# Performance work log

Measured on AMD Instinct MI355X. Metric: run time of the kernel, lower is better.

Reference implementation:

```python
import jax, jax.numpy as jnp
import numpy as np

N_NODES = 50000
N_EDGES = 500000
IN_DIM = 512
HID = 512


def setup_inputs() -> dict:
    key = jax.random.key(0)
    ks = jax.random.split(key, 12)
    s = 0.02  # weight init scale
    x = jax.random.normal(ks[0], (N_NODES, IN_DIM), dtype=jnp.float32)
    edge_index = jax.random.randint(ks[1], (2, N_EDGES), 0, N_NODES, dtype=jnp.int32)
    return {
        "x": x,
        "edge_index": edge_index,
        "Wl0": jax.random.normal(ks[2], (IN_DIM, HID), jnp.float32) * s,
        "bl0": jnp.zeros((HID,), jnp.float32),
        "Wr0": jax.random.normal(ks[3], (IN_DIM, HID), jnp.float32) * s,
        "Wl1": jax.random.normal(ks[4], (HID, HID), jnp.float32) * s,
        "bl1": jnp.zeros((HID,), jnp.float32),
        "Wr1": jax.random.normal(ks[5], (HID, HID), jnp.float32) * s,
        "Wv": jax.random.normal(ks[6], (HID, HID), jnp.float32) * s,
        "bv": jnp.zeros((HID,), jnp.float32),
        "Wt": jax.random.normal(ks[7], (HID, HID), jnp.float32) * s,
        "bt": jnp.zeros((HID,), jnp.float32),
    }


def _sage_conv(x, src, dst, Wl, bl, Wr, n_nodes):
    # mean-aggregate source features at target nodes, then dual linear
    msg_sum = jax.ops.segment_sum(x[src], dst, num_segments=n_nodes)  # [N, d]
    deg = jax.ops.segment_sum(jnp.ones_like(dst, dtype=x.dtype), dst, num_segments=n_nodes)
    mean = msg_sum / jnp.maximum(deg, 1.0)[:, None]
    return mean @ Wl + bl + x @ Wr


def reference(x, edge_index, Wl0, bl0, Wr0, Wl1, bl1, Wr1, Wv, bv, Wt, bt):
    n = x.shape[0]
    src, dst = edge_index[0], edge_index[1]
    h = _sage_conv(x, src, dst, Wl0, bl0, Wr0, n)
    h = jax.nn.relu(h)  # dropout is identity in eval mode
    h = _sage_conv(h, src, dst, Wl1, bl1, Wr1, n)
    x_vision = jax.nn.relu(h @ Wv + bv)
    x_text = jax.nn.relu(h @ Wt + bt)
    return (h, x_vision, x_text)
```

## Files before the change

kernel.cpp:

```cpp
#include <hip/hip_runtime.h>
#include <hip/hip_bf16.h>
#include <stdint.h>

#define N_NODES 50000
#define N_EDGES 500000
#define DIM 512

typedef unsigned short u16;
typedef unsigned int u32;
typedef __bf16 bf16x8 __attribute__((ext_vector_type(8)));
typedef float f32x4 __attribute__((ext_vector_type(4)));

static __device__ __forceinline__ u16 f2bf(float f) {
  union { __bf16 b; u16 u; } cv; cv.b = (__bf16)f; return cv.u;
}
static __device__ __forceinline__ float bf2f(u16 u) {
  union { u16 u; __bf16 b; } cv; cv.u = u; return (float)cv.b;
}

__global__ void k_zero(int4* __restrict__ deg4) {
  int t = blockIdx.x * 256 + threadIdx.x;
  if (t < 12500) deg4[t] = make_int4(0, 0, 0, 0);
}

__global__ __launch_bounds__(1024) void k_scan(const int* __restrict__ deg,
                                               int* __restrict__ offs,
                                               int* __restrict__ pos,
                                               float* __restrict__ invd) {
  __shared__ int sums[1024];
  const int tid = threadIdx.x;
  const int CH = 49;
  int lo = tid * CH;
  int hi = lo + CH; if (hi > N_NODES) hi = N_NODES;
  if (lo > N_NODES) lo = N_NODES;
  int s = 0;
  for (int i = lo; i < hi; ++i) s += deg[i];
  sums[tid] = s;
  __syncthreads();
  for (int off = 1; off < 1024; off <<= 1) {
    int t = (tid >= off) ? sums[tid - off] : 0;
    __syncthreads();
    sums[tid] += t;
    __syncthreads();
  }
  int run = sums[tid] - s;
  for (int i = lo; i < hi; ++i) {
    int d = deg[i];
    offs[i] = run; pos[i] = run;
    invd[i] = 1.0f / (float)((d > 1) ? d : 1);
    run += d;
  }
  if (tid == 1023) offs[N_NODES] = run;
}

__global__ void k_scatter(const int* __restrict__ src, const int* __restrict__ dst,
                          int* __restrict__ pos, int* __restrict__ srcs) {
  int e = blockIdx.x * blockDim.x + threadIdx.x;
  if (e < N_EDGES) {
    int p = atomicAdd(&pos[dst[e]], 1);
    srcs[p] = src[e] * DIM;
  }
}

__global__ __launch_bounds__(256) void k_prep(
    const float* __restrict__ x, u16* __restrict__ xb,
    const int* __restrict__ dst, int* __restrict__ deg,
    const float* __restrict__ Wa, const float* __restrict__ Wb,
    const float* __restrict__ Wc, const float* __restrict__ Wd,
    const float* __restrict__ We, const float* __restrict__ Wf,
    u16* __restrict__ Oa, u16* __restrict__ Ob, u16* __restrict__ Oc,
    u16* __restrict__ Od, u16* __restrict__ Oe, u16* __restrict__ Of) {
  __shared__ u16 tbuf[64][66];
  const int t = blockIdx.x * 256 + threadIdx.x;

  const float4* p = (const float4*)(x + (size_t)t * 8);
  float4 a = p[0], b = p[1];
  uint4 o;
  o.x = (u32)f2bf(a.x) | ((u32)f2bf(a.y) << 16);
  o.y = (u32)f2bf(a.z) | ((u32)f2bf(a.w) << 16);
  o.z = (u32)f2bf(b.x) | ((u32)f2bf(b.y) << 16);
  o.w = (u32)f2bf(b.z) | ((u32)f2bf(b.w) << 16);
  *(uint4*)(xb + (size_t)t * 8) = o;

  if (t < N_EDGES) atomicAdd(&deg[dst[t]], 1);

  const int wb = (int)blockIdx.x - (12500 - 384);
  if (wb >= 0) {
    const float* W; u16* O;
    switch (wb / 64) {
      case 0: W = Wa; O = Oa; break;
      case 1: W = Wb; O = Ob; break;
      case 2: W = Wc; O = Oc; break;
      case 3: W = Wd; O = Od; break;
      case 4: W = We; O = Oe; break;
      default: W = Wf; O = Of; break;
    }
    const int rem = wb & 63;
    const int k0 = (rem & 7) * 64, n0 = (rem >> 3) * 64;
    const int lr = threadIdx.x & 63, wr = threadIdx.x >> 6;
#pragma unroll
    for (int rr = 0; rr < 16; ++rr) {
      int k = k0 + wr * 16 + rr;
      tbuf[lr][wr * 16 + rr] = f2bf(W[(size_t)k * 512 + n0 + lr]);
    }
    __syncthreads();
#pragma unroll
    for (int rr = 0; rr < 16; ++rr) {
      int n = n0 + wr * 16 + rr;
      O[(size_t)n * 512 + k0 + lr] = tbuf[wr * 16 + rr][lr];
    }
  }
}

#define ACCB(A, q)                                              \
  A[0] += bf2f((q).x & 0xffff); A[1] += bf2f((u16)((q).x >> 16)); \
  A[2] += bf2f((q).y & 0xffff); A[3] += bf2f((u16)((q).y >> 16)); \
  A[4] += bf2f((q).z & 0xffff); A[5] += bf2f((u16)((q).z >> 16)); \
  A[6] += bf2f((q).w & 0xffff); A[7] += bf2f((u16)((q).w >> 16));

__global__ __launch_bounds__(256) void k_agg_bf16(
    const u16* __restrict__ hb, const int* __restrict__ offs,
    const int* __restrict__ srcs, const float* __restrict__ invd,
    u16* __restrict__ outb) {
  int node = blockIdx.x * 4 + (threadIdx.x >> 6);
  int lane = threadIdx.x & 63;
  if (node >= N_NODES) return;
  int s0 = offs[node], s1 = offs[node + 1];
  float acc[8] = {0, 0, 0, 0, 0, 0, 0, 0};
  float acd[8] = {0, 0, 0, 0, 0, 0, 0, 0};
  const u16* hl = hb + lane * 8;
  int i = s0;
  for (; i + 8 <= s1; i += 8) {
    int sa = srcs[i], sb = srcs[i + 1], sc = srcs[i + 2], sd = srcs[i + 3];
    int se = srcs[i + 4], sf = srcs[i + 5], sg = srcs[i + 6], sh = srcs[i + 7];
    uint4 qa = *(const uint4*)(hl + sa);
    uint4 qb = *(const uint4*)(hl + sb);
    uint4 qc = *(const uint4*)(hl + sc);
    uint4 qd = *(const uint4*)(hl + sd);
    uint4 qe = *(const uint4*)(hl + se);
    uint4 qf = *(const uint4*)(hl + sf);
    uint4 qg = *(const uint4*)(hl + sg);
    uint4 qh = *(const uint4*)(hl + sh);
    ACCB(acc, qa) ACCB(acd, qb) ACCB(acc, qc) ACCB(acd, qd)
    ACCB(acc, qe) ACCB(acd, qf) ACCB(acc, qg) ACCB(acd, qh)
  }
  if (i + 4 <= s1) {
    int sa = srcs[i], sb = srcs[i + 1], sc = srcs[i + 2], sd = srcs[i + 3];
    uint4 qa = *(const uint4*)(hl + sa);
    uint4 qb = *(const uint4*)(hl + sb);
    uint4 qc = *(const uint4*)(hl + sc);
    uint4 qd = *(const uint4*)(hl + sd);
    ACCB(acc, qa) ACCB(acd, qb) ACCB(acc, qc) ACCB(acd, qd)
    i += 4;
  }
  if (i + 2 <= s1) {
    int sa = srcs[i], sb = srcs[i + 1];
    uint4 qa = *(const uint4*)(hl + sa);
    uint4 qb = *(const uint4*)(hl + sb);
    ACCB(acc, qa) ACCB(acd, qb)
    i += 2;
  }
  if (i < s1) {
    int sa = srcs[i];
    uint4 qa = *(const uint4*)(hl + sa);
    ACCB(acc, qa)
  }
  float iv = invd[node];
#pragma unroll
  for (int k = 0; k < 8; ++k) acc[k] = (acc[k] + acd[k]) * iv;
  uint4 o;
  o.x = (u32)f2bf(acc[0]) | ((u32)f2bf(acc[1]) << 16);
  o.y = (u32)f2bf(acc[2]) | ((u32)f2bf(acc[3]) << 16);
  o.z = (u32)f2bf(acc[4]) | ((u32)f2bf(acc[5]) << 16);
  o.w = (u32)f2bf(acc[6]) | ((u32)f2bf(acc[7]) << 16);
  *(uint4*)(outb + (size_t)node * DIM + lane * 8) = o;
}

#define MFMA __builtin_amdgcn_mfma_f32_16x16x32_bf16
#define BUFU 39936

template <int EPI>
__global__ __launch_bounds__(512, 2) void k_gemm112(
    const u16* __restrict__ A1, const u16* __restrict__ W1,
    const u16* __restrict__ A2, const u16* __restrict__ W2,
    const float* __restrict__ bias, const float* __restrict__ bias2,
    float* __restrict__ outf, float* __restrict__ outf2,
    u16* __restrict__ outb, int NT) {
  __shared__ u16 lds[2 * BUFU];
  const int tid = threadIdx.x;
  const int wid = tid >> 6, lane = tid & 63;
  int head = 0, row0;
  if (EPI == 3) {
    head = (int)blockIdx.x & 1;
    row0 = ((int)blockIdx.x >> 1) * 112;
  } else {
    row0 = (int)blockIdx.x * 112;
  }
  const u16* BW = (EPI == 3) ? (head ? W2 : W1) : nullptr;

  f32x4 acc[7][4];
  const f32x4 z = {0.f, 0.f, 0.f, 0.f};
#pragma unroll
  for (int i = 0; i < 7; ++i)
#pragma unroll
    for (int j = 0; j < 4; ++j) acc[i][j] = z;

  const int ly = lane >> 3;
  const int schunk = (lane & 7) ^ ly;

  auto stageA = [&](int t, int h) {
    u16* tile = lds + (t & 1) * BUFU;
    const u16* G = (EPI == 3) ? A1 : ((t < 8) ? A1 : A2);
    int w = wid;
    if (h && w >= 6) w -= 2;
    const int rb = h * 64 + w * 8;
    int rg = row0 + rb + ly;
    if (rg > N_NODES - 1) rg = N_NODES - 1;
    const u16* g = G + (size_t)rg * 512 + (t & 7) * 64 + schunk * 8;
    __builtin_amdgcn_global_load_lds(
        (const __attribute__((address_space(1))) void*)g,
        (__attribute__((address_space(3))) void*)(tile + rb * 64), 16, 0, 0);
  };

  auto stageB = [&](int t, int jh) {
    u16* tile = lds + (t & 1) * BUFU + 7168;
    const u16* G = (EPI == 3) ? BW : ((t < 8) ? W1 : W2);
    const int kofs = (t & 7) * 64 + schunk * 8;
#pragma unroll
    for (int u = 0; u < 4; ++u) {
      const int rb = u * 128 + (wid >> 2) * 64 + (wid & 3) * 8 + jh * 32;
      const u16* g = G + (size_t)(rb + ly) * 512 + kofs;
      __builtin_amdgcn_global_load_lds(
          (const __attribute__((address_space(1))) void*)g,
          (__attribute__((address_space(3))) void*)(tile + rb * 64), 16, 0, 0);
    }
  };

  auto rdA = [&](const u16* T_, int ig, int kk) -> bf16x8 {
    const int r = ig * 16 + (lane & 15);
    const int off = ((kk * 4 + (lane >> 4)) ^ (lane & 7)) * 8;
    return *(const bf16x8*)(T_ + r * 64 + off);
  };
  auto rdB = [&](const u16* T_, int jg, int kk) -> bf16x8 {
    const int r = wid * 64 + jg * 16 + (lane & 15);
    const int off = ((kk * 4 + (lane >> 4)) ^ (lane & 7)) * 8;
    return *(const bf16x8*)(T_ + r * 64 + off);
  };

  stageA(0, 0); stageB(0, 0); stageB(0, 1); stageA(0, 1);

  for (int t = 0; t < NT; ++t) {
    const u16* At = lds + (t & 1) * BUFU;
    const u16* Bt = At + 7168;
    const bool more = (t + 1 < NT);
    bf16x8 aF[4][2], bF[2][2];

    asm volatile("s_waitcnt vmcnt(5)" ::: "memory");
    __builtin_amdgcn_s_barrier();
    asm volatile("" ::: "memory");
    if (more) stageA(t + 1, 0);
#pragma unroll
    for (int ip = 0; ip < 4; ++ip)
#pragma unroll
      for (int kk = 0; kk < 2; ++kk) aF[ip][kk] = rdA(At, ip, kk);
#pragma unroll
    for (int jp = 0; jp < 2; ++jp)
#pragma unroll
      for (int kk = 0; kk < 2; ++kk) bF[jp][kk] = rdB(Bt, jp, kk);
    __builtin_amdgcn_s_setprio(1);
#pragma unroll
    for (int ip = 0; ip < 4; ++ip)
#pragma unroll
      for (int jp = 0; jp < 2; ++jp)
#pragma unroll
        for (int kk = 0; kk < 2; ++kk)
          acc[ip][jp] = MFMA(aF[ip][kk], bF[jp][kk], acc[ip][jp], 0, 0, 0);
    __builtin_amdgcn_s_setprio(0);

    if (more) { asm volatile("s_waitcnt vmcnt(1)" ::: "memory"); }
    else      { asm volatile("s_waitcnt vmcnt(0)" ::: "memory"); }
    __builtin_amdgcn_s_barrier();
    asm volatile("" ::: "memory");
    if (more) stageB(t + 1, 0);
#pragma unroll
    for (int jp = 0; jp < 2; ++jp)
#pragma unroll
      for (int kk = 0; kk < 2; ++kk) bF[jp][kk] = rdB(Bt, 2 + jp, kk);
    __builtin_amdgcn_s_setprio(1);
#pragma unroll
    for (int ip = 0; ip < 4; ++ip)
#pragma unroll
      for (int jp = 0; jp < 2; ++jp)
#pragma unroll
        for (int kk = 0; kk < 2; ++kk)
          acc[ip][2 + jp] = MFMA(aF[ip][kk], bF[jp][kk], acc[ip][2 + jp], 0, 0, 0);
    __builtin_amdgcn_s_setprio(0);

    if (more) stageB(t + 1, 1);
#pragma unroll
    for (int ip = 0; ip < 3; ++ip)
#pragma unroll
      for (int kk = 0; kk < 2; ++kk) aF[ip][kk] = rdA(At, 4 + ip, kk);
    __builtin_amdgcn_s_setprio(1);
#pragma unroll
    for (int ip = 0; ip < 3; ++ip)
#pragma unroll
      for (int jp = 0; jp < 2; ++jp)
#pragma unroll
        for (int kk = 0; kk < 2; ++kk)
          acc[4 + ip][2 + jp] = MFMA(aF[ip][kk], bF[jp][kk], acc[4 + ip][2 + jp], 0, 0, 0);
    __builtin_amdgcn_s_setprio(0);

    if (more) stageA(t + 1, 1);
#pragma unroll
    for (int jp = 0; jp < 2; ++jp)
#pragma unroll
      for (int kk = 0; kk < 2; ++kk) bF[jp][kk] = rdB(Bt, jp, kk);
    __builtin_amdgcn_s_setprio(1);
#pragma unroll
    for (int ip = 0; ip < 3; ++ip)
#pragma unroll
      for (int jp = 0; jp < 2; ++jp)
#pragma unroll
        for (int kk = 0; kk < 2; ++kk)
          acc[4 + ip][jp] = MFMA(aF[ip][kk], bF[jp][kk], acc[4 + ip][jp], 0, 0, 0);
    __builtin_amdgcn_s_setprio(0);
  }

  const float* bs = (EPI == 3 && head) ? bias2 : bias;
  float* of = (EPI == 3 && head) ? outf2 : outf;
#pragma unroll
  for (int jg = 0; jg < 4; ++jg) {
    int col = wid * 64 + jg * 16 + (lane & 15);
    float bb = bs[col];
#pragma unroll
    for (int ig = 0; ig < 7; ++ig) {
      int rbase = row0 + ig * 16 + (lane >> 4) * 4;
      f32x4 v = acc[ig][jg];
#pragma unroll
      for (int r = 0; r < 4; ++r) {
        int row = rbase + r;
        if (row < N_NODES) {
          float f = v[r] + bb;
          if (EPI == 0) {
            f = fmaxf(f, 0.f);
            outb[(size_t)row * DIM + col] = f2bf(f);
          } else if (EPI == 1) {
            outf[(size_t)row * DIM + col] = f;
            outb[(size_t)row * DIM + col] = f2bf(f);
          } else {
            of[(size_t)row * DIM + col] = fmaxf(f, 0.f);
          }
        }
      }
    }
  }
}

extern "C" void kernel_launch(void* const* d_in, const int* in_sizes, int n_in,
                              void* d_out, int out_size, void* d_ws, size_t ws_size,
                              hipStream_t stream) {
  (void)in_sizes; (void)n_in; (void)out_size; (void)ws_size;
  const float* x   = (const float*)d_in[0];
  const int*   ei  = (const int*)d_in[1];
  const float* Wl0 = (const float*)d_in[2];
  const float* bl0 = (const float*)d_in[3];
  const float* Wr0 = (const float*)d_in[4];
  const float* Wl1 = (const float*)d_in[5];
  const float* bl1 = (const float*)d_in[6];
  const float* Wr1 = (const float*)d_in[7];
  const float* Wv  = (const float*)d_in[8];
  const float* bv  = (const float*)d_in[9];
  const float* Wt  = (const float*)d_in[10];
  const float* bt  = (const float*)d_in[11];
  const int* srcI = ei;
  const int* dstI = ei + N_EDGES;

  float* out_h = (float*)d_out;
  float* out_v = out_h + (size_t)N_NODES * DIM;
  float* out_t = out_v + (size_t)N_NODES * DIM;
  u16* meanb  = (u16*)out_v;
  u16* hrelub = (u16*)out_t;

  uint8_t* p = (uint8_t*)d_ws;
  auto carve = [&](size_t bytes) -> uint8_t* {
    uint8_t* r = p; p += (bytes + 1023) & ~(size_t)1023; return r;
  };
  int*   deg  = (int*)carve((size_t)N_NODES * 4);
  int*   offs = (int*)carve((size_t)(N_NODES + 1) * 4);
  int*   pos  = (int*)carve((size_t)N_NODES * 4);
  float* invd = (float*)carve((size_t)N_NODES * 4);
  int*   srcs = (int*)carve((size_t)N_EDGES * 4);
  u16* Wl0b = (u16*)carve(512 * 512 * 2);
  u16* Wr0b = (u16*)carve(512 * 512 * 2);
  u16* Wl1b = (u16*)carve(512 * 512 * 2);
  u16* Wr1b = (u16*)carve(512 * 512 * 2);
  u16* Wvb  = (u16*)carve(512 * 512 * 2);
  u16* Wtb  = (u16*)carve(512 * 512 * 2);
  u16* xb   = (u16*)carve((size_t)N_NODES * DIM * 2);

  const int EB = (N_EDGES + 255) / 256;

  k_zero<<<49, 256, 0, stream>>>((int4*)deg);

  k_prep<<<12500, 256, 0, stream>>>(x, xb, dstI, deg,
                                    Wl0, Wr0, Wl1, Wr1, Wv, Wt,
                                    Wl0b, Wr0b, Wl1b, Wr1b, Wvb, Wtb);
  k_scan<<<1, 1024, 0, stream>>>(deg, offs, pos, invd);
  k_scatter<<<EB, 256, 0, stream>>>(srcI, dstI, pos, srcs);

  const int GB = 448;

  k_agg_bf16<<<12500, 256, 0, stream>>>(xb, offs, srcs, invd, meanb);
  k_gemm112<0><<<GB, 512, 0, stream>>>(meanb, Wl0b, xb, Wr0b, bl0, nullptr,
                                       nullptr, nullptr, hrelub, 16);

  k_agg_bf16<<<12500, 256, 0, stream>>>(hrelub, offs, srcs, invd, meanb);
  k_gemm112<1><<<GB, 512, 0, stream>>>(meanb, Wl1b, hrelub, Wr1b, bl1, nullptr,
                                       out_h, nullptr, xb, 16);

  k_gemm112<3><<<896, 512, 0, stream>>>(xb, Wvb, nullptr, Wtb, bv, bt,
                                        out_v, out_t, nullptr, 8);
}
```

Before: 646.7 us.

## Fuse neighbor mean aggregation into SAGE GEMM via LDS-resident mean tile

Replaces the separate aggregation kernel and dual GEMM with one kernel per SAGE layer. Each block gathers mean features for 80 nodes into a swizzled LDS tile, then runs MFMA over the mean tile and the root features. The weights are streamed into double-buffered LDS with global_load_lds. This drops the bf16 mean round trip through global memory and one launch per layer. In exchange the per-block LDS use (about 144KB) limits occupancy, the gather phase cannot overlap with the MFMA phase inside a block, and the weight tiles are reloaded by all 625 blocks.

```diff
diff --git a/kernel.cpp b/kernel.cpp
--- a/kernel.cpp
+++ b/kernel.cpp
@@ -118,65 +118,176 @@
   A[4] += bf2f((q).z & 0xffff); A[5] += bf2f((u16)((q).z >> 16)); \
   A[6] += bf2f((q).w & 0xffff); A[7] += bf2f((u16)((q).w >> 16));
 
-__global__ __launch_bounds__(256) void k_agg_bf16(
-    const u16* __restrict__ hb, const int* __restrict__ offs,
+#define MFMA __builtin_amdgcn_mfma_f32_16x16x32_bf16
+
+template <int EPI>
+__global__ __launch_bounds__(512, 2) void k_fused(
+    const u16* __restrict__ Ain, const u16* __restrict__ WL,
+    const u16* __restrict__ WR, const int* __restrict__ offs,
     const int* __restrict__ srcs, const float* __restrict__ invd,
+    const float* __restrict__ bias, float* __restrict__ outf,
     u16* __restrict__ outb) {
-  int node = blockIdx.x * 4 + (threadIdx.x >> 6);
-  int lane = threadIdx.x & 63;
-  if (node >= N_NODES) return;
-  int s0 = offs[node], s1 = offs[node + 1];
-  float acc[8] = {0, 0, 0, 0, 0, 0, 0, 0};
-  float acd[8] = {0, 0, 0, 0, 0, 0, 0, 0};
-  const u16* hl = hb + lane * 8;
-  int i = s0;
-  for (; i + 8 <= s1; i += 8) {
-    int sa = srcs[i], sb = srcs[i + 1], sc = srcs[i + 2], sd = srcs[i + 3];
-    int se = srcs[i + 4], sf = srcs[i + 5], sg = srcs[i + 6], sh = srcs[i + 7];
-    uint4 qa = *(const uint4*)(hl + sa);
-    uint4 qb = *(const uint4*)(hl + sb);
-    uint4 qc = *(const uint4*)(hl + sc);
-    uint4 qd = *(const uint4*)(hl + sd);
-    uint4 qe = *(const uint4*)(hl + se);
-    uint4 qf = *(const uint4*)(hl + sf);
-    uint4 qg = *(const uint4*)(hl + sg);
-    uint4 qh = *(const uint4*)(hl + sh);
-    ACCB(acc, qa) ACCB(acd, qb) ACCB(acc, qc) ACCB(acd, qd)
-    ACCB(acc, qe) ACCB(acd, qf) ACCB(acc, qg) ACCB(acd, qh)
-  }
-  if (i + 4 <= s1) {
-    int sa = srcs[i], sb = srcs[i + 1], sc = srcs[i + 2], sd = srcs[i + 3];
-    uint4 qa = *(const uint4*)(hl + sa);
-    uint4 qb = *(const uint4*)(hl + sb);
-    uint4 qc = *(const uint4*)(hl + sc);
-    uint4 qd = *(const uint4*)(hl + sd);
-    ACCB(acc, qa) ACCB(acd, qb) ACCB(acc, qc) ACCB(acd, qd)
-    i += 4;
-  }
-  if (i + 2 <= s1) {
-    int sa = srcs[i], sb = srcs[i + 1];
-    uint4 qa = *(const uint4*)(hl + sa);
-    uint4 qb = *(const uint4*)(hl + sb);
-    ACCB(acc, qa) ACCB(acd, qb)
-    i += 2;
-  }
-  if (i < s1) {
-    int sa = srcs[i];
-    uint4 qa = *(const uint4*)(hl + sa);
-    ACCB(acc, qa)
-  }
-  float iv = invd[node];
-#pragma unroll
-  for (int k = 0; k < 8; ++k) acc[k] = (acc[k] + acd[k]) * iv;
-  uint4 o;
-  o.x = (u32)f2bf(acc[0]) | ((u32)f2bf(acc[1]) << 16);
-  o.y = (u32)f2bf(acc[2]) | ((u32)f2bf(acc[3]) << 16);
-  o.z = (u32)f2bf(acc[4]) | ((u32)f2bf(acc[5]) << 16);
-  o.w = (u32)f2bf(acc[6]) | ((u32)f2bf(acc[7]) << 16);
-  *(uint4*)(outb + (size_t)node * DIM + lane * 8) = o;
-}
-
-#define MFMA __builtin_amdgcn_mfma_f32_16x16x32_bf16
+  __shared__ u16 meanA[80 * 512];
+  __shared__ u16 Bbuf[2][16384];
+  const int tid = threadIdx.x;
+  const int wid = tid >> 6, lane = tid & 63;
+  const int row0 = (int)blockIdx.x * 80;
+
+  const u16* hl = Ain + lane * 8;
+  for (int j = 0; j < 10; ++j) {
+    const int nl = wid * 10 + j;
+    const int node = row0 + nl;
+    const int s0 = offs[node], s1 = offs[node + 1];
+    float ac0[8] = {0, 0, 0, 0, 0, 0, 0, 0};
+    float ac1[8] = {0, 0, 0, 0, 0, 0, 0, 0};
+    int i = s0;
+    for (; i + 8 <= s1; i += 8) {
+      int sa = srcs[i], sb = srcs[i + 1], sc = srcs[i + 2], sd = srcs[i + 3];
+      int se = srcs[i + 4], sf = srcs[i + 5], sg = srcs[i + 6], sh = srcs[i + 7];
+      uint4 qa = *(const uint4*)(hl + sa);
+      uint4 qb = *(const uint4*)(hl + sb);
+      uint4 qc = *(const uint4*)(hl + sc);
+      uint4 qd = *(const uint4*)(hl + sd);
+      uint4 qe = *(const uint4*)(hl + se);
+      uint4 qf = *(const uint4*)(hl + sf);
+      uint4 qg = *(const uint4*)(hl + sg);
+      uint4 qh = *(const uint4*)(hl + sh);
+      ACCB(ac0, qa) ACCB(ac1, qb) ACCB(ac0, qc) ACCB(ac1, qd)
+      ACCB(ac0, qe) ACCB(ac1, qf) ACCB(ac0, qg) ACCB(ac1, qh)
+    }
+    if (i + 4 <= s1) {
+      int sa = srcs[i], sb = srcs[i + 1], sc = srcs[i + 2], sd = srcs[i + 3];
+      uint4 qa = *(const uint4*)(hl + sa);
+      uint4 qb = *(const uint4*)(hl + sb);
+      uint4 qc = *(const uint4*)(hl + sc);
+      uint4 qd = *(const uint4*)(hl + sd);
+      ACCB(ac0, qa) ACCB(ac1, qb) ACCB(ac0, qc) ACCB(ac1, qd)
+      i += 4;
+    }
+    if (i + 2 <= s1) {
+      int sa = srcs[i], sb = srcs[i + 1];
+      uint4 qa = *(const uint4*)(hl + sa);
+      uint4 qb = *(const uint4*)(hl + sb);
+      ACCB(ac0, qa) ACCB(ac1, qb)
+      i += 2;
+    }
+    if (i < s1) {
+      int sa = srcs[i];
+      uint4 qa = *(const uint4*)(hl + sa);
+      ACCB(ac0, qa)
+    }
+    const float iv = invd[node];
+#pragma unroll
+    for (int k = 0; k < 8; ++k) ac0[k] = (ac0[k] + ac1[k]) * iv;
+    uint4 w;
+    w.x = (u32)f2bf(ac0[0]) | ((u32)f2bf(ac0[1]) << 16);
+    w.y = (u32)f2bf(ac0[2]) | ((u32)f2bf(ac0[3]) << 16);
+    w.z = (u32)f2bf(ac0[4]) | ((u32)f2bf(ac0[5]) << 16);
+    w.w = (u32)f2bf(ac0[6]) | ((u32)f2bf(ac0[7]) << 16);
+    *(uint4*)(meanA + (size_t)nl * 512 + ((lane ^ (nl & 7)) << 3)) = w;
+  }
+
+  f32x4 acc[5][4];
+  const f32x4 z = {0.f, 0.f, 0.f, 0.f};
+#pragma unroll
+  for (int i = 0; i < 5; ++i)
+#pragma unroll
+    for (int j = 0; j < 4; ++j) acc[i][j] = z;
+
+  auto stageB = [&](int tt) {
+    const u16* G = (tt < 16) ? WL : WR;
+    const int kbase = (tt & 15) * 32;
+    u16* dst0 = &Bbuf[tt & 1][0];
+    const int swz = (lane & 3) ^ ((lane >> 3) & 3);
+#pragma unroll
+    for (int p = 0; p < 4; ++p) {
+      const int sb = (p * 8 + wid) * 64;
+      const int r = (sb >> 2) + (lane >> 2);
+      const u16* g = G + (size_t)r * 512 + kbase + (swz << 3);
+      __builtin_amdgcn_global_load_lds(
+          (const __attribute__((address_space(1))) void*)g,
+          (__attribute__((address_space(3))) void*)(dst0 + (size_t)sb * 8),
+          16, 0, 0);
+    }
+  };
+
+  uint4 aN[5], aC[5];
+  auto loadA2 = [&](int tt) {
+    const int kbase = (tt - 16) * 32 + ((lane >> 4) << 3);
+#pragma unroll
+    for (int i = 0; i < 5; ++i) {
+      const int row = row0 + i * 16 + (lane & 15);
+      aN[i] = *(const uint4*)(Ain + (size_t)row * 512 + kbase);
+    }
+  };
+
+  stageB(0);
+
+  for (int t = 0; t < 32; ++t) {
+    asm volatile("s_waitcnt vmcnt(0)" ::: "memory");
+    __builtin_amdgcn_s_barrier();
+    asm volatile("" ::: "memory");
+    if (t >= 16) {
+#pragma unroll
+      for (int i = 0; i < 5; ++i) aC[i] = aN[i];
+    }
+    if (t + 1 < 32) {
+      stageB(t + 1);
+      if (t + 1 >= 16) loadA2(t + 1);
+    }
+
+    bf16x8 aF[5], bF[4];
+    const u16* Bt = &Bbuf[t & 1][0];
+#pragma unroll
+    for (int jg = 0; jg < 4; ++jg) {
+      const int cc = wid * 64 + jg * 16 + (lane & 15);
+      const int slot = cc * 4 + ((lane >> 4) ^ ((cc >> 1) & 3));
+      bF[jg] = *(const bf16x8*)(Bt + (size_t)slot * 8);
+    }
+    if (t < 16) {
+      const int kc = t * 4 + (lane >> 4);
+#pragma unroll
+      for (int ig = 0; ig < 5; ++ig) {
+        const int r = ig * 16 + (lane & 15);
+        aF[ig] = *(const bf16x8*)(meanA + (size_t)r * 512 + ((kc ^ (r & 7)) << 3));
+      }
+    } else {
+#pragma unroll
+      for (int ig = 0; ig < 5; ++ig) aF[ig] = *(const bf16x8*)&aC[ig];
+    }
+    __builtin_amdgcn_s_setprio(1);
+#pragma unroll
+    for (int ig = 0; ig < 5; ++ig)
+#pragma unroll
+      for (int jg = 0; jg < 4; ++jg)
+        acc[ig][jg] = MFMA(aF[ig], bF[jg], acc[ig][jg], 0, 0, 0);
+    __builtin_amdgcn_s_setprio(0);
+  }
+
+#pragma unroll
+  for (int jg = 0; jg < 4; ++jg) {
+    const int col = wid * 64 + jg * 16 + (lane & 15);
+    const float bb = bias[col];
+#pragma unroll
+    for (int ig = 0; ig < 5; ++ig) {
+      const int rbase = row0 + ig * 16 + ((lane >> 4) << 2);
+      f32x4 v = acc[ig][jg];
+#pragma unroll
+      for (int r = 0; r < 4; ++r) {
+        const int row = rbase + r;
+        float f = v[r] + bb;
+        if (EPI == 0) {
+          f = fmaxf(f, 0.f);
+          outb[(size_t)row * DIM + col] = f2bf(f);
+        } else {
+          outf[(size_t)row * DIM + col] = f;
+          outb[(size_t)row * DIM + col] = f2bf(f);
+        }
+      }
+    }
+  }
+}
+
 #define BUFU 39936
 
 template <int EPI>
@@ -379,7 +490,6 @@
   float* out_h = (float*)d_out;
   float* out_v = out_h + (size_t)N_NODES * DIM;
   float* out_t = out_v + (size_t)N_NODES * DIM;
-  u16* meanb  = (u16*)out_v;
   u16* hrelub = (u16*)out_t;
 
   uint8_t* p = (uint8_t*)d_ws;
@@ -402,23 +512,16 @@
   const int EB = (N_EDGES + 255) / 256;
 
   k_zero<<<49, 256, 0, stream>>>((int4*)deg);
-
   k_prep<<<12500, 256, 0, stream>>>(x, xb, dstI, deg,
                                     Wl0, Wr0, Wl1, Wr1, Wv, Wt,
                                     Wl0b, Wr0b, Wl1b, Wr1b, Wvb, Wtb);
   k_scan<<<1, 1024, 0, stream>>>(deg, offs, pos, invd);
   k_scatter<<<EB, 256, 0, stream>>>(srcI, dstI, pos, srcs);
 
-  const int GB = 448;
-
-  k_agg_bf16<<<12500, 256, 0, stream>>>(xb, offs, srcs, invd, meanb);
-  k_gemm112<0><<<GB, 512, 0, stream>>>(meanb, Wl0b, xb, Wr0b, bl0, nullptr,
-                                       nullptr, nullptr, hrelub, 16);
-
-  k_agg_bf16<<<12500, 256, 0, stream>>>(hrelub, offs, srcs, invd, meanb);
-  k_gemm112<1><<<GB, 512, 0, stream>>>(meanb, Wl1b, hrelub, Wr1b, bl1, nullptr,
-                                       out_h, nullptr, xb, 16);
-
+  k_fused<0><<<625, 512, 0, stream>>>(xb, Wl0b, Wr0b, offs, srcs, invd,
+                                      bl0, nullptr, hrelub);
+  k_fused<1><<<625, 512, 0, stream>>>(hrelub, Wl1b, Wr1b, offs, srcs, invd,
+                                      bl1, out_h, xb);
   k_gemm112<3><<<896, 512, 0, stream>>>(xb, Wvb, nullptr, Wtb, bv, bt,
                                         out_v, out_t, nullptr, 8);
 }
```

After: 827.4 us. 1.28x slower.

## Replace 112-row GEMM tile with 80-row tile using K=32 stages

Applied to the files above, without the earlier changes.

Rewrites the fused dual GEMM kernel to use 80-row by 512-column block tiles with 32-wide K slices, a simpler single-barrier double-buffered pipeline, and a new LDS swizzle. 80 divides 50000 exactly, so the kernel drops row clamping and bounds checks and avoids wasted padded rows, using 625 blocks instead of 448. In exchange it halves the K step, doubling the number of barriers and the global-to-LDS staging overhead per output. It also waits on all outstanding loads every iteration, which reduces overlap of loads with MFMA work.

```diff
diff --git a/kernel.cpp b/kernel.cpp
--- a/kernel.cpp
+++ b/kernel.cpp
@@ -177,153 +177,97 @@
 }
 
 #define MFMA __builtin_amdgcn_mfma_f32_16x16x32_bf16
-#define BUFU 39936
 
 template <int EPI>
-__global__ __launch_bounds__(512, 2) void k_gemm112(
+__global__ __launch_bounds__(512, 2) void k_g2(
     const u16* __restrict__ A1, const u16* __restrict__ W1,
     const u16* __restrict__ A2, const u16* __restrict__ W2,
     const float* __restrict__ bias, const float* __restrict__ bias2,
     float* __restrict__ outf, float* __restrict__ outf2,
     u16* __restrict__ outb, int NT) {
-  __shared__ u16 lds[2 * BUFU];
+  __shared__ u16 Abuf[2][2560];
+  __shared__ u16 Bbuf[2][16384];
   const int tid = threadIdx.x;
   const int wid = tid >> 6, lane = tid & 63;
   int head = 0, row0;
   if (EPI == 3) {
     head = (int)blockIdx.x & 1;
-    row0 = ((int)blockIdx.x >> 1) * 112;
+    row0 = ((int)blockIdx.x >> 1) * 80;
   } else {
-    row0 = (int)blockIdx.x * 112;
+    row0 = (int)blockIdx.x * 80;
   }
   const u16* BW = (EPI == 3) ? (head ? W2 : W1) : nullptr;
 
-  f32x4 acc[7][4];
+  f32x4 acc[5][4];
   const f32x4 z = {0.f, 0.f, 0.f, 0.f};
 #pragma unroll
-  for (int i = 0; i < 7; ++i)
+  for (int i = 0; i < 5; ++i)
 #pragma unroll
     for (int j = 0; j < 4; ++j) acc[i][j] = z;
 
-  const int ly = lane >> 3;
-  const int schunk = (lane & 7) ^ ly;
-
-  auto stageA = [&](int t, int h) {
-    u16* tile = lds + (t & 1) * BUFU;
-    const u16* G = (EPI == 3) ? A1 : ((t < 8) ? A1 : A2);
-    int w = wid;
-    if (h && w >= 6) w -= 2;
-    const int rb = h * 64 + w * 8;
-    int rg = row0 + rb + ly;
-    if (rg > N_NODES - 1) rg = N_NODES - 1;
-    const u16* g = G + (size_t)rg * 512 + (t & 7) * 64 + schunk * 8;
-    __builtin_amdgcn_global_load_lds(
-        (const __attribute__((address_space(1))) void*)g,
-        (__attribute__((address_space(3))) void*)(tile + rb * 64), 16, 0, 0);
-  };
-
-  auto stageB = [&](int t, int jh) {
-    u16* tile = lds + (t & 1) * BUFU + 7168;
-    const u16* G = (EPI == 3) ? BW : ((t < 8) ? W1 : W2);
-    const int kofs = (t & 7) * 64 + schunk * 8;
-#pragma unroll
-    for (int u = 0; u < 4; ++u) {
-      const int rb = u * 128 + (wid >> 2) * 64 + (wid & 3) * 8 + jh * 32;
-      const u16* g = G + (size_t)(rb + ly) * 512 + kofs;
+  const int swz = (lane & 3) ^ ((lane >> 3) & 3);
+
+  auto stageA = [&](int t) {
+    if (wid < 5) {
+      const u16* G = (EPI == 3) ? A1 : ((t < 16) ? A1 : A2);
+      const int r = wid * 16 + (lane >> 2);
+      const u16* g = G + (size_t)(row0 + r) * 512 + (t & 15) * 32 + (swz << 3);
       __builtin_amdgcn_global_load_lds(
           (const __attribute__((address_space(1))) void*)g,
-          (__attribute__((address_space(3))) void*)(tile + rb * 64), 16, 0, 0);
-    }
-  };
-
-  auto rdA = [&](const u16* T_, int ig, int kk) -> bf16x8 {
+          (__attribute__((address_space(3))) void*)(&Abuf[t & 1][0] +
+                                                    (size_t)(wid * 64) * 8),
+          16, 0, 0);
+    }
+  };
+
+  auto stageB = [&](int t) {
+    const u16* G = (EPI == 3) ? BW : ((t < 16) ? W1 : W2);
+    const int kbase = (t & 15) * 32;
+    u16* dst0 = &Bbuf[t & 1][0];
+#pragma unroll
+    for (int p = 0; p < 4; ++p) {
+      const int sb = (p * 8 + wid) * 64;
+      const int r = (sb >> 2) + (lane >> 2);
+      const u16* g = G + (size_t)r * 512 + kbase + (swz << 3);
+      __builtin_amdgcn_global_load_lds(
+          (const __attribute__((address_space(1))) void*)g,
+          (__attribute__((address_space(3))) void*)(dst0 + (size_t)sb * 8),
+          16, 0, 0);
+    }
+  };
+
+  auto rdA = [&](const u16* T_, int ig) -> bf16x8 {
     const int r = ig * 16 + (lane & 15);
-    const int off = ((kk * 4 + (lane >> 4)) ^ (lane & 7)) * 8;
-    return *(const bf16x8*)(T_ + r * 64 + off);
-  };
-  auto rdB = [&](const u16* T_, int jg, int kk) -> bf16x8 {
-    const int r = wid * 64 + jg * 16 + (lane & 15);
-    const int off = ((kk * 4 + (lane >> 4)) ^ (lane & 7)) * 8;
-    return *(const bf16x8*)(T_ + r * 64 + off);
-  };
-
-  stageA(0, 0); stageB(0, 0); stageB(0, 1); stageA(0, 1);
+    const int slot = (lane >> 4) ^ ((r >> 1) & 3);
+    return *(const bf16x8*)(T_ + r * 32 + slot * 8);
+  };
+  auto rdB = [&](const u16* T_, int jg) -> bf16x8 {
+    const int cc = wid * 64 + jg * 16 + (lane & 15);
+    const int slot = (lane >> 4) ^ ((cc >> 1) & 3);
+    return *(const bf16x8*)(T_ + cc * 32 + slot * 8);
+  };
+
+  stageA(0); stageB(0);
 
   for (int t = 0; t < NT; ++t) {
-    const u16* At = lds + (t & 1) * BUFU;
-    const u16* Bt = At + 7168;
-    const bool more = (t + 1 < NT);
-    bf16x8 aF[4][2], bF[2][2];
-
-    asm volatile("s_waitcnt vmcnt(5)" ::: "memory");
+    asm volatile("s_waitcnt vmcnt(0)" ::: "memory");
     __builtin_amdgcn_s_barrier();
     asm volatile("" ::: "memory");
-    if (more) stageA(t + 1, 0);
-#pragma unroll
-    for (int ip = 0; ip < 4; ++ip)
-#pragma unroll
-      for (int kk = 0; kk < 2; ++kk) aF[ip][kk] = rdA(At, ip, kk);
-#pragma unroll
-    for (int jp = 0; jp < 2; ++jp)
-#pragma unroll
-      for (int kk = 0; kk < 2; ++kk) bF[jp][kk] = rdB(Bt, jp, kk);
+    if (t + 1 < NT) { stageA(t + 1); stageB(t + 1); }
+
+    bf16x8 aF[5], bF[4];
+    const u16* At = &Abuf[t & 1][0];
+    const u16* Bt = &Bbuf[t & 1][0];
+#pragma unroll
+    for (int ig = 0; ig < 5; ++ig) aF[ig] = rdA(At, ig);
+#pragma unroll
+    for (int jg = 0; jg < 4; ++jg) bF[jg] = rdB(Bt, jg);
     __builtin_amdgcn_s_setprio(1);
 #pragma unroll
-    for (int ip = 0; ip < 4; ++ip)
-#pragma unroll
-      for (int jp = 0; jp < 2; ++jp)
-#pragma unroll
-        for (int kk = 0; kk < 2; ++kk)
-          acc[ip][jp] = MFMA(aF[ip][kk], bF[jp][kk], acc[ip][jp], 0, 0, 0);
-    __builtin_amdgcn_s_setprio(0);
-
-    if (more) { asm volatile("s_waitcnt vmcnt(1)" ::: "memory"); }
-    else      { asm volatile("s_waitcnt vmcnt(0)" ::: "memory"); }
-    __builtin_amdgcn_s_barrier();
-    asm volatile("" ::: "memory");
-    if (more) stageB(t + 1, 0);
-#pragma unroll
-    for (int jp = 0; jp < 2; ++jp)
-#pragma unroll
-      for (int kk = 0; kk < 2; ++kk) bF[jp][kk] = rdB(Bt, 2 + jp, kk);
-    __builtin_amdgcn_s_setprio(1);
-#pragma unroll
-    for (int ip = 0; ip < 4; ++ip)
-#pragma unroll
-      for (int jp = 0; jp < 2; ++jp)
-#pragma unroll
-        for (int kk = 0; kk < 2; ++kk)
-          acc[ip][2 + jp] = MFMA(aF[ip][kk], bF[jp][kk], acc[ip][2 + jp], 0, 0, 0);
-    __builtin_amdgcn_s_setprio(0);
-
-    if (more) stageB(t + 1, 1);
-#pragma unroll
-    for (int ip = 0; ip < 3; ++ip)
-#pragma unroll
-      for (int kk = 0; kk < 2; ++kk) aF[ip][kk] = rdA(At, 4 + ip, kk);
-    __builtin_amdgcn_s_setprio(1);
-#pragma unroll
-    for (int ip = 0; ip < 3; ++ip)
-#pragma unroll
-      for (int jp = 0; jp < 2; ++jp)
-#pragma unroll
-        for (int kk = 0; kk < 2; ++kk)
-          acc[4 + ip][2 + jp] = MFMA(aF[ip][kk], bF[jp][kk], acc[4 + ip][2 + jp], 0, 0, 0);
-    __builtin_amdgcn_s_setprio(0);
-
-    if (more) stageA(t + 1, 1);
-#pragma unroll
-    for (int jp = 0; jp < 2; ++jp)
-#pragma unroll
-      for (int kk = 0; kk < 2; ++kk) bF[jp][kk] = rdB(Bt, jp, kk);
-    __builtin_amdgcn_s_setprio(1);
-#pragma unroll
-    for (int ip = 0; ip < 3; ++ip)
-#pragma unroll
-      for (int jp = 0; jp < 2; ++jp)
-#pragma unroll
-        for (int kk = 0; kk < 2; ++kk)
-          acc[4 + ip][jp] = MFMA(aF[ip][kk], bF[jp][kk], acc[4 + ip][jp], 0, 0, 0);
+    for (int ig = 0; ig < 5; ++ig)
+#pragma unroll
+      for (int jg = 0; jg < 4; ++jg)
+        acc[ig][jg] = MFMA(aF[ig], bF[jg], acc[ig][jg], 0, 0, 0);
     __builtin_amdgcn_s_setprio(0);
   }
 
@@ -331,26 +275,24 @@
   float* of = (EPI == 3 && head) ? outf2 : outf;
 #pragma unroll
   for (int jg = 0; jg < 4; ++jg) {
-    int col = wid * 64 + jg * 16 + (lane & 15);
-    float bb = bs[col];
-#pragma unroll
-    for (int ig = 0; ig < 7; ++ig) {
-      int rbase = row0 + ig * 16 + (lane >> 4) * 4;
+    const int col = wid * 64 + jg * 16 + (lane & 15);
+    const float bb = bs[col];
+#pragma unroll
+    for (int ig = 0; ig < 5; ++ig) {
+      const int rbase = row0 + ig * 16 + ((lane >> 4) << 2);
       f32x4 v = acc[ig][jg];
 #pragma unroll
       for (int r = 0; r < 4; ++r) {
-        int row = rbase + r;
-        if (row < N_NODES) {
-          float f = v[r] + bb;
-          if (EPI == 0) {
-            f = fmaxf(f, 0.f);
-            outb[(size_t)row * DIM + col] = f2bf(f);
-          } else if (EPI == 1) {
-            outf[(size_t)row * DIM + col] = f;
-            outb[(size_t)row * DIM + col] = f2bf(f);
-          } else {
-            of[(size_t)row * DIM + col] = fmaxf(f, 0.f);
-          }
+        const int row = rbase + r;
+        float f = v[r] + bb;
+        if (EPI == 0) {
+          f = fmaxf(f, 0.f);
+          outb[(size_t)row * DIM + col] = f2bf(f);
+        } else if (EPI == 1) {
+          outf[(size_t)row * DIM + col] = f;
+          outb[(size_t)row * DIM + col] = f2bf(f);
+        } else {
+          of[(size_t)row * DIM + col] = fmaxf(f, 0.f);
         }
       }
     }
@@ -402,23 +344,20 @@
   const int EB = (N_EDGES + 255) / 256;
 
   k_zero<<<49, 256, 0, stream>>>((int4*)deg);
-
   k_prep<<<12500, 256, 0, stream>>>(x, xb, dstI, deg,
                                     Wl0, Wr0, Wl1, Wr1, Wv, Wt,
                                     Wl0b, Wr0b, Wl1b, Wr1b, Wvb, Wtb);
   k_scan<<<1, 1024, 0, stream>>>(deg, offs, pos, invd);
   k_scatter<<<EB, 256, 0, stream>>>(srcI, dstI, pos, srcs);
 
-  const int GB = 448;
-
   k_agg_bf16<<<12500, 256, 0, stream>>>(xb, offs, srcs, invd, meanb);
-  k_gemm112<0><<<GB, 512, 0, stream>>>(meanb, Wl0b, xb, Wr0b, bl0, nullptr,
-                                       nullptr, nullptr, hrelub, 16);
+  k_g2<0><<<625, 512, 0, stream>>>(meanb, Wl0b, xb, Wr0b, bl0, nullptr,
+                                   nullptr, nullptr, hrelub, 32);
 
   k_agg_bf16<<<12500, 256, 0, stream>>>(hrelub, offs, srcs, invd, meanb);
-  k_gemm112<1><<<GB, 512, 0, stream>>>(meanb, Wl1b, hrelub, Wr1b, bl1, nullptr,
-                                       out_h, nullptr, xb, 16);
-
-  k_gemm112<3><<<896, 512, 0, stream>>>(xb, Wvb, nullptr, Wtb, bv, bt,
-                                        out_v, out_t, nullptr, 8);
-}
+  k_g2<1><<<625, 512, 0, stream>>>(meanb, Wl1b, hrelub, Wr1b, bl1, nullptr,
+                                   out_h, nullptr, xb, 32);
+
+  k_g2<3><<<1250, 512, 0, stream>>>(xb, Wvb, nullptr, Wtb, bv, bt,
+                                    out_v, out_t, nullptr, 16);
+}
```

Measured after the change: 729.0 us. +12.7%, slower.
